# Performance work log

Hardware: AMD Instinct MI355X
Metric: run time of the kernel (lower is better)

Reference implementation:

```python
import jax, jax.numpy as jnp
import numpy as np

EPS_NORM = 1e-8
EPS_REG = 1e-6

def _l2_normalize(x, eps=EPS_NORM):
    return x / jnp.clip(jnp.linalg.norm(x, axis=-1, keepdims=True), eps, None)

def setup_inputs() -> dict:
    key = jax.random.key(0)
    k1, k2, k3, k4 = jax.random.split(key, 4)
    ns, nq, d, C = 16384, 8192, 256, 64
    return {
        "support_features": jax.random.normal(k1, (ns, d), dtype=jnp.float32),
        "support_labels": jax.random.randint(k2, (ns,), 0, C),
        "support_values": jax.random.normal(k3, (ns,), dtype=jnp.float32),
        "query_features": jax.random.normal(k4, (nq, d), dtype=jnp.float32),
        "num_classes": C,
    }

def reference(support_features, support_labels, support_values, query_features, num_classes):
    # ---- forward_classification: cosine-sim prototypes ----
    sf = _l2_normalize(support_features)            # [ns, d]
    qf = _l2_normalize(query_features)              # [nq, d]
    sums = jax.ops.segment_sum(sf, support_labels, num_segments=num_classes)   # [C, d]
    counts = jax.ops.segment_sum(jnp.ones((sf.shape[0],), sf.dtype),
                                 support_labels, num_segments=num_classes)      # [C]
    prototypes = _l2_normalize(sums / jnp.clip(counts, 1.0, None)[:, None])     # [C, d]
    logits = qf @ prototypes.T                      # [nq, C]
    log_probs = jax.nn.log_softmax(logits, axis=1)

    mu = support_features.mean(axis=0, keepdims=True)           # [1, d]
    S = support_features - mu                                   # [ns, d]
    ns, d = S.shape
    cov = (S.T @ S) / max(ns - 1, 1) + 1e-4 * jnp.eye(d, dtype=S.dtype)
    evals, evecs = jnp.linalg.eigh(cov)
    inv_sqrt = (evecs * jax.lax.rsqrt(jnp.clip(evals, 1e-6, None))) @ evecs.T   # [d, d]
    S_wh = S @ inv_sqrt                                          # [ns, d]
    Q_wh = (query_features - mu) @ inv_sqrt                      # [nq, d]
    # squared euclidean cdist: [nq, ns]
    d2 = jnp.clip(jnp.sum(Q_wh * Q_wh, axis=1)[:, None]
                  + jnp.sum(S_wh * S_wh, axis=1)[None, :]
                  - 2.0 * (Q_wh @ S_wh.T), 0.0, None)
    med = jnp.median(d2)
    gamma = jnp.where(jnp.isfinite(med) & (med > 0),
                      1.0 / (med + EPS_REG),
                      1.0 / (d2.mean() + EPS_REG))
    weights = jax.nn.softmax(-gamma * d2, axis=1)                # [nq, ns]
    prediction = weights @ support_values                        # [nq]
    return log_probs, prediction
```

## Files before the change

### kernel.cpp

```cpp
#include <hip/hip_runtime.h>
#include <hip/hip_bf16.h>

constexpr int kNS = 16384;
constexpr int kNQ = 8192;
constexpr int kD  = 256;
constexpr int kC  = 64;


constexpr size_t OFF_PSUM  = 0;
constexpr size_t OFF_HIST  = 82240;
constexpr size_t OFF_SSUM  = 84288;
constexpr size_t OFF_MU    = 100736;
constexpr size_t OFF_COV   = 100992;
constexpr size_t OFF_C     = 166784;
constexpr size_t OFF_Y     = 166800;
constexpr size_t OFF_T     = 297872;
constexpr size_t OFF_Y2    = 363408;
constexpr size_t OFF_S2    = 560016;
constexpr size_t OFF_Q2P   = 576400;
constexpr size_t OFF_PART  = 584592;
constexpr size_t OFF_G     = 846736;
constexpr size_t OFF_SH    = 2943888;
constexpr size_t OFF_GH    = 5041040;

typedef __attribute__((ext_vector_type(8))) short bf16x8;
typedef __attribute__((ext_vector_type(4))) float f32x4;

__device__ __forceinline__ unsigned short f2bf(float f) {
  unsigned int w; __builtin_memcpy(&w, &f, 4);
  unsigned int r = (w + 0x7FFFu + ((w >> 16) & 1u)) >> 16;
  return (unsigned short)r;
}

__device__ __forceinline__ float waveReduceSum(float v) {
#pragma unroll
  for (int off = 32; off > 0; off >>= 1) v += __shfl_xor(v, off);
  return v;
}
__device__ __forceinline__ float waveReduceMax(float v) {
#pragma unroll
  for (int off = 32; off > 0; off >>= 1) v = fmaxf(v, __shfl_xor(v, off));
  return v;
}
__device__ __forceinline__ void fma16(float acc[4][4], float4 a, float4 b) {
  acc[0][0] += a.x*b.x; acc[0][1] += a.x*b.y; acc[0][2] += a.x*b.z; acc[0][3] += a.x*b.w;
  acc[1][0] += a.y*b.x; acc[1][1] += a.y*b.y; acc[1][2] += a.y*b.z; acc[1][3] += a.y*b.w;
  acc[2][0] += a.z*b.x; acc[2][1] += a.z*b.y; acc[2][2] += a.z*b.z; acc[2][3] += a.z*b.w;
  acc[3][0] += a.w*b.x; acc[3][1] += a.w*b.y; acc[3][2] += a.w*b.z; acc[3][3] += a.w*b.w;
}

__device__ __forceinline__ void gload_lds16(const void* g, void* l) {
  __builtin_amdgcn_global_load_lds(
      (const __attribute__((address_space(1))) unsigned int*)g,
      (__attribute__((address_space(3))) unsigned int*)l, 16, 0, 0);
}

__global__ void k_swzs_r27(const float* __restrict__ in, unsigned short* __restrict__ out,
                           float* __restrict__ rnorm, float* __restrict__ ws) {
  int gid = blockIdx.x * 256 + threadIdx.x;
  if (gid < 2049) ws[OFF_HIST + gid] = 0.f;
  else if (gid < 2049 + 8192) ws[OFF_Q2P + (gid - 2049)] = 0.f;
  else if (gid < 2049 + 8192 + 16384) ws[OFF_S2 + (gid - 2049 - 8192)] = 0.f;

  __shared__ float rs[16];
  int g = blockIdx.x, t = threadIdx.x;
  if (t < 16) rs[t] = 0.f;
  __syncthreads();
  int ks = t >> 5;
  float4 va[2], vb[2];
#pragma unroll
  for (int f = 0; f < 2; ++f) {
    int lane = (2 * t + f) & 63;
    int q = lane >> 4, r = lane & 15;
    const float* src = &in[(size_t)(g * 16 + r) * kD + ks * 32 + q * 8];
    va[f] = *(const float4*)src;
    vb[f] = *(const float4*)(src + 4);
    float s = va[f].x*va[f].x + va[f].y*va[f].y + va[f].z*va[f].z + va[f].w*va[f].w
            + vb[f].x*vb[f].x + vb[f].y*vb[f].y + vb[f].z*vb[f].z + vb[f].w*vb[f].w;
    atomicAdd(&rs[r], s);
  }
  size_t gbase = (size_t)g * 4096;
#pragma unroll
  for (int f = 0; f < 2; ++f) {
    int lane = (2 * t + f) & 63;
    ushort4 o0, o1;
    o0.x = f2bf(va[f].x); o0.y = f2bf(va[f].y); o0.z = f2bf(va[f].z); o0.w = f2bf(va[f].w);
    o1.x = f2bf(vb[f].x); o1.y = f2bf(vb[f].y); o1.z = f2bf(vb[f].z); o1.w = f2bf(vb[f].w);
    unsigned short* dst = &out[gbase + (size_t)ks * 512 + (size_t)lane * 8];
    *(ushort4*)dst = o0;
    *(ushort4*)(dst + 4) = o1;
  }
  __syncthreads();
  if (t < 16) rnorm[g * 16 + t] = 1.0f / fmaxf(sqrtf(rs[t]), 1e-8f);
}

__global__ void k_paccum_r24(const float* __restrict__ X, const int* __restrict__ lab,
                             const float* __restrict__ rnorm,
                             float* __restrict__ partial, float* __restrict__ cntpart,
                             float* __restrict__ cpart) {
  __shared__ float acc[kC * kD];
  int t = threadIdx.x, b = blockIdx.x;
  for (int i = t; i < kC * kD; i += 256) acc[i] = 0.f;
  __syncthreads();
  int r0 = b * 128;
  float myCnt = 0.f, csum = 0.f;
  for (int r = 0; r < 128; r += 8) {
    int row = r0 + r;
    int   c0 = lab[row + 0], c1 = lab[row + 1], c2 = lab[row + 2], c3 = lab[row + 3];
    int   c4 = lab[row + 4], c5 = lab[row + 5], c6 = lab[row + 6], c7 = lab[row + 7];
    float n0 = rnorm[row + 0], n1 = rnorm[row + 1], n2 = rnorm[row + 2], n3 = rnorm[row + 3];
    float n4 = rnorm[row + 4], n5 = rnorm[row + 5], n6 = rnorm[row + 6], n7 = rnorm[row + 7];
    float x0 = X[(size_t)(row + 0) * kD + t];
    float x1 = X[(size_t)(row + 1) * kD + t];
    float x2 = X[(size_t)(row + 2) * kD + t];
    float x3 = X[(size_t)(row + 3) * kD + t];
    float x4 = X[(size_t)(row + 4) * kD + t];
    float x5 = X[(size_t)(row + 5) * kD + t];
    float x6 = X[(size_t)(row + 6) * kD + t];
    float x7 = X[(size_t)(row + 7) * kD + t];
    csum += ((x0 + x1) + (x2 + x3)) + ((x4 + x5) + (x6 + x7));
    acc[c0 * kD + t] += x0 * n0;
    acc[c1 * kD + t] += x1 * n1;
    acc[c2 * kD + t] += x2 * n2;
    acc[c3 * kD + t] += x3 * n3;
    acc[c4 * kD + t] += x4 * n4;
    acc[c5 * kD + t] += x5 * n5;
    acc[c6 * kD + t] += x6 * n6;
    acc[c7 * kD + t] += x7 * n7;
    myCnt += (t == c0) ? 1.f : 0.f; myCnt += (t == c1) ? 1.f : 0.f;
    myCnt += (t == c2) ? 1.f : 0.f; myCnt += (t == c3) ? 1.f : 0.f;
    myCnt += (t == c4) ? 1.f : 0.f; myCnt += (t == c5) ? 1.f : 0.f;
    myCnt += (t == c6) ? 1.f : 0.f; myCnt += (t == c7) ? 1.f : 0.f;
  }
  __syncthreads();
  float* pb = partial + (size_t)b * (kC * kD);
  for (int c = 0; c < kC; ++c) pb[c * kD + t] = acc[c * kD + t];
  if (t < kC) cntpart[b * kC + t] = myCnt;
  cpart[(size_t)b * kD + t] = csum;
}

__global__ void k_proto_fin_r28(const float* __restrict__ partial,
                                const float* __restrict__ cntpart,
                                const float* __restrict__ cpart,
                                unsigned short* __restrict__ Ph,
                                float* __restrict__ mu) {
  int c = blockIdx.x, t = threadIdx.x;
  if (c == kC) {
    float s = 0.f;
    for (int b = 0; b < 128; ++b) s += cpart[(size_t)b * kD + t];
    mu[t] = s * (1.0f / (float)kNS);
    return;
  }
  __shared__ float cs[128];
  __shared__ float wred[4];
  __shared__ float cntS, invS;
  if (t < 128) cs[t] = cntpart[t * kC + c];
  __syncthreads();
  float s = 0.f;
  const float* p = partial + (size_t)c * kD + t;
  for (int b = 0; b < 128; ++b) s += p[(size_t)b * (kC * kD)];
  if (t < 64) {
    float cv = cs[t] + cs[t + 64];
    cv = waveReduceSum(cv);
    if (t == 0) cntS = fmaxf(cv, 1.0f);
  }
  __syncthreads();
  float v = s / cntS;
  float ss = waveReduceSum(v * v);
  if ((t & 63) == 0) wred[t >> 6] = ss;
  __syncthreads();
  if (t == 0) invS = 1.0f / fmaxf(sqrtf(wred[0] + wred[1] + wred[2] + wred[3]), 1e-8f);
  __syncthreads();
  float val = v * invS;
  int g = c >> 4, r = c & 15;
  int ks = t >> 5, q = (t >> 3) & 3, j = t & 7;
  Ph[(size_t)g * 4096 + (size_t)ks * 512 + (size_t)(q * 16 + r) * 8 + j] = f2bf(val);
}

__global__ void k_qlogits_r28(const float* __restrict__ Q,
                              const unsigned short* __restrict__ Ph,
                              float* __restrict__ out0) {
  __shared__ float rs[16];
  __shared__ alignas(16) unsigned short qtile[16][264];
  int g = blockIdx.x, t = threadIdx.x;
  if (t < 16) rs[t] = 0.f;
  __syncthreads();
  int ks0 = t >> 5;
  float4 va[2], vb[2];
  int rr[2], cc[2];
#pragma unroll
  for (int f = 0; f < 2; ++f) {
    int lane = (2 * t + f) & 63;
    int q8 = lane >> 4, r = lane & 15;
    rr[f] = r; cc[f] = ks0 * 32 + q8 * 8;
    const float* src = &Q[(size_t)(g * 16 + r) * kD + cc[f]];
    va[f] = *(const float4*)src;
    vb[f] = *(const float4*)(src + 4);
    float s = va[f].x*va[f].x + va[f].y*va[f].y + va[f].z*va[f].z + va[f].w*va[f].w
            + vb[f].x*vb[f].x + vb[f].y*vb[f].y + vb[f].z*vb[f].z + vb[f].w*vb[f].w;
    atomicAdd(&rs[r], s);
  }
  __syncthreads();
#pragma unroll
  for (int f = 0; f < 2; ++f) {
    float n = 1.0f / fmaxf(sqrtf(rs[rr[f]]), 1e-8f);
    ushort4 o0, o1;
    o0.x = f2bf(va[f].x * n); o0.y = f2bf(va[f].y * n);
    o0.z = f2bf(va[f].z * n); o0.w = f2bf(va[f].w * n);
    o1.x = f2bf(vb[f].x * n); o1.y = f2bf(vb[f].y * n);
    o1.z = f2bf(vb[f].z * n); o1.w = f2bf(vb[f].w * n);
    unsigned short* dst = &qtile[rr[f]][cc[f]];
    *(ushort4*)dst = o0;
    *(ushort4*)(dst + 4) = o1;
  }
  __syncthreads();
  if (t >= 64) return;

  int lane = t, l15 = lane & 15, quad = lane >> 4;
  bf16x8 afrag[8];
#pragma unroll
  for (int ks = 0; ks < 8; ++ks)
    afrag[ks] = *(const bf16x8*)&qtile[l15][ks * 32 + quad * 8];

  f32x4 acc0 = {0.f,0.f,0.f,0.f}, acc1 = {0.f,0.f,0.f,0.f};
  f32x4 acc2 = {0.f,0.f,0.f,0.f}, acc3 = {0.f,0.f,0.f,0.f};
#pragma unroll
  for (int ks = 0; ks < 8; ++ks) {
    bf16x8 b0 = *(const bf16x8*)&Ph[(size_t)0 * 4096 + ks * 512 + (size_t)lane * 8];
    bf16x8 b1 = *(const bf16x8*)&Ph[(size_t)1 * 4096 + ks * 512 + (size_t)lane * 8];
    bf16x8 b2 = *(const bf16x8*)&Ph[(size_t)2 * 4096 + ks * 512 + (size_t)lane * 8];
    bf16x8 b3 = *(const bf16x8*)&Ph[(size_t)3 * 4096 + ks * 512 + (size_t)lane * 8];
    acc0 = __builtin_amdgcn_mfma_f32_16x16x32_bf16(afrag[ks], b0, acc0, 0, 0, 0);
    acc1 = __builtin_amdgcn_mfma_f32_16x16x32_bf16(afrag[ks], b1, acc1, 0, 0, 0);
    acc2 = __builtin_amdgcn_mfma_f32_16x16x32_bf16(afrag[ks], b2, acc2, 0, 0, 0);
    acc3 = __builtin_amdgcn_mfma_f32_16x16x32_bf16(afrag[ks], b3, acc3, 0, 0, 0);
  }
#pragma unroll
  for (int r = 0; r < 4; ++r) {
    float m = fmaxf(fmaxf(acc0[r], acc1[r]), fmaxf(acc2[r], acc3[r]));
#pragma unroll
    for (int off = 8; off >= 1; off >>= 1) m = fmaxf(m, __shfl_xor(m, off));
    float e = expf(acc0[r] - m) + expf(acc1[r] - m) + expf(acc2[r] - m) + expf(acc3[r] - m);
#pragma unroll
    for (int off = 8; off >= 1; off >>= 1) e += __shfl_xor(e, off);
    float lse = m + logf(e);
    size_t row = (size_t)g * 16 + quad * 4 + r;
    out0[row * kC + 0 * 16 + l15] = acc0[r] - lse;
    out0[row * kC + 1 * 16 + l15] = acc1[r] - lse;
    out0[row * kC + 2 * 16 + l15] = acc2[r] - lse;
    out0[row * kC + 3 * 16 + l15] = acc3[r] - lse;
  }
}

__global__ void k_xtx_r26(const float* __restrict__ X, float* __restrict__ part) {
  const int TA[10] = {0,0,0,0,1,1,1,2,2,3};
  const int TB[10] = {0,1,2,3,1,2,3,2,3,3};
  __shared__ alignas(16) float As[16][68];
  __shared__ alignas(16) float Bs[16][68];
  int t = threadIdx.x, tx = t & 15, ty = t >> 4;
  int ab = TA[blockIdx.x] * 64, bb = TB[blockIdx.x] * 64;
  int k0b = blockIdx.y * 512;
  float acc[4][4] = {};
  for (int k0 = 0; k0 < 512; k0 += 16) {
    __syncthreads();
    int j = t & 63, kr0 = t >> 6;
#pragma unroll
    for (int p = 0; p < 4; ++p) {
      int kr = kr0 + p * 4;
      size_t base = (size_t)(k0b + k0 + kr) * kD;
      As[kr][j] = X[base + ab + j];
      Bs[kr][j] = X[base + bb + j];
    }
    __syncthreads();
#pragma unroll
    for (int k = 0; k < 16; ++k) {
      float4 a = *(const float4*)&As[k][ty * 4];
      float4 b = *(const float4*)&Bs[k][tx * 4];
      fma16(acc, a, b);
    }
  }
  float* pb = part + ((size_t)blockIdx.y * 10 + blockIdx.x) * 4096;
#pragma unroll
  for (int r = 0; r < 4; ++r) {
    float4 o = {acc[r][0], acc[r][1], acc[r][2], acc[r][3]};
    *(float4*)&pb[(size_t)(ty * 4 + r) * 64 + tx * 4] = o;
  }
}

__global__ void k_xtxcov_r28(const float* __restrict__ part, const float* __restrict__ mu,
                             float* __restrict__ cov, float* __restrict__ X1) {
  int i = blockIdx.x, j = threadIdx.x;
  int a = i >> 6, b = j >> 6;
  int tile, local;
  if (a <= b) { tile = a * (9 - a) / 2 + (b - a); local = (i & 63) * 64 + (j & 63); }
  else        { tile = b * (9 - b) / 2 + (a - b); local = (j & 63) * 64 + (i & 63); }
  const float* p = part + (size_t)tile * 4096 + local;
  float s = 0.f;
#pragma unroll 8
  for (int ky = 0; ky < 32; ++ky) s += p[(size_t)ky * 40960];
  float v = (s - (float)kNS * mu[i] * mu[j]) * (1.0f / (float)(kNS - 1));
  if (i == j) v += 1e-4f;
  cov[(size_t)i * kD + j] = v;
  X1[(size_t)i * kD + j] = (i == j ? 2.0f : 0.0f) - v;
}

__global__ void __launch_bounds__(1024)
k_newt_mm_r17(const float* __restrict__ A, const float* __restrict__ Xin,
              float* __restrict__ Out, int isT) {
  __shared__ float a_s[256];
  __shared__ float red[3][256];
  int i = blockIdx.x, t = threadIdx.x;
  int j = t & 255, kq = t >> 8;
  if (t < 256) a_s[t] = A[(size_t)i * kD + t];
  __syncthreads();
  int k0 = kq * 64;
  const float* Xp = &Xin[(size_t)k0 * kD + j];
  float s0 = 0.f, s1 = 0.f, s2 = 0.f, s3 = 0.f;
#pragma unroll 4
  for (int k = 0; k < 64; k += 4) {
    s0 = fmaf(a_s[k0 + k + 0], Xp[0 * kD], s0);
    s1 = fmaf(a_s[k0 + k + 1], Xp[1 * kD], s1);
    s2 = fmaf(a_s[k0 + k + 2], Xp[2 * kD], s2);
    s3 = fmaf(a_s[k0 + k + 3], Xp[3 * kD], s3);
    Xp += 4 * kD;
  }
  float s = (s0 + s1) + (s2 + s3);
  if (kq) red[kq - 1][j] = s;
  __syncthreads();
  if (t < 256) {
    float tot = s + red[0][j] + red[1][j] + red[2][j];
    float o = isT ? ((i == j ? 2.0f : 0.0f) - tot) : tot;
    Out[(size_t)i * kD + j] = o;
  }
}

__global__ void k_G_r26(const float* __restrict__ Q, const float* __restrict__ mu,
                        const float* __restrict__ M, float* __restrict__ G,
                        unsigned short* __restrict__ Gh, float* __restrict__ q2p) {
  __shared__ alignas(16) float As[16][68];
  __shared__ alignas(16) float Bs[16][68];
  int t = threadIdx.x, tx = t & 15, ty = t >> 4;
  int nb = blockIdx.x * 64;
  int mb = blockIdx.y * 64;
  float acc[4][4] = {};
  for (int k0 = 0; k0 < 256; k0 += 16) {
    __syncthreads();
    {
      int kk = t & 15, m0 = t >> 4;
      float muk = mu[k0 + kk];
#pragma unroll
      for (int p = 0; p < 4; ++p) {
        int m = m0 + p * 16;
        As[kk][m] = Q[(size_t)(mb + m) * kD + k0 + kk] - muk;
      }
      int j = t & 63, kr0 = t >> 6;
#pragma unroll
      for (int p = 0; p < 4; ++p) {
        int kr = kr0 + p * 4;
        Bs[kr][j] = M[(size_t)(k0 + kr) * kD + nb + j];
      }
    }
    __syncthreads();
#pragma unroll
    for (int k = 0; k < 16; ++k) {
      float4 a = *(const float4*)&As[k][ty * 4];
      float4 b = *(const float4*)&Bs[k][tx * 4];
      fma16(acc, a, b);
    }
  }
  int d0 = nb + tx * 4;
  int ks = d0 >> 5, q = (d0 >> 3) & 3, j0 = d0 & 7;
#pragma unroll
  for (int r = 0; r < 4; ++r) {
    int gi = mb + ty * 4 + r;
    float4 o = {acc[r][0], acc[r][1], acc[r][2], acc[r][3]};
    *(float4*)&G[(size_t)gi * kD + nb + tx * 4] = o;
    int gg = gi >> 4, rrow = gi & 15;
    ushort4 h;
    h.x = f2bf(acc[r][0]); h.y = f2bf(acc[r][1]);
    h.z = f2bf(acc[r][2]); h.w = f2bf(acc[r][3]);
    *(ushort4*)&Gh[(size_t)gg * 4096 + (size_t)ks * 512 + (size_t)(q * 16 + rrow) * 8 + j0] = h;
    const float* qr = &Q[(size_t)gi * kD + d0];
    float p = acc[r][0] * (qr[0] + mu[d0 + 0]) + acc[r][1] * (qr[1] + mu[d0 + 1])
            + acc[r][2] * (qr[2] + mu[d0 + 2]) + acc[r][3] * (qr[3] + mu[d0 + 3]);
#pragma unroll
    for (int off = 8; off >= 1; off >>= 1) p += __shfl_xor(p, off);
    if (tx == 0) atomicAdd(&q2p[gi], p);
  }
}

__global__ void k_s2_r26(const float* __restrict__ S, const float* __restrict__ mu,
                         const float* __restrict__ M, float* __restrict__ s2) {
  __shared__ alignas(16) float As[16][68];
  __shared__ alignas(16) float Bs[16][68];
  __shared__ float red[64][17];
  int t = threadIdx.x, tx = t & 15, ty = t >> 4;
  int mb = blockIdx.x * 64;
  int nb = blockIdx.y * 64;
  float partial[4] = {0.f, 0.f, 0.f, 0.f};
  float acc[4][4] = {};
  for (int k0 = 0; k0 < 256; k0 += 16) {
    __syncthreads();
    {
      int kk = t & 15, m0 = t >> 4;
      float muk = mu[k0 + kk];
#pragma unroll
      for (int p = 0; p < 4; ++p) {
        int m = m0 + p * 16;
        As[kk][m] = S[(size_t)(mb + m) * kD + k0 + kk] - muk;
      }
      int j = t & 63, kr0 = t >> 6;
#pragma unroll
      for (int p = 0; p < 4; ++p) {
        int kr = kr0 + p * 4;
        Bs[kr][j] = M[(size_t)(k0 + kr) * kD + nb + j];
      }
    }
    __syncthreads();
#pragma unroll
    for (int k = 0; k < 16; ++k) {
      float4 a = *(const float4*)&As[k][ty * 4];
      float4 b = *(const float4*)&Bs[k][tx * 4];
      fma16(acc, a, b);
    }
  }
#pragma unroll
  for (int r = 0; r < 4; ++r) {
    int gi = mb + ty * 4 + r;
#pragma unroll
    for (int c = 0; c < 4; ++c) {
      int gj = nb + tx * 4 + c;
      partial[r] += acc[r][c] * (S[(size_t)gi * kD + gj] - mu[gj]);
    }
  }
  __syncthreads();
#pragma unroll
  for (int r = 0; r < 4; ++r) red[ty * 4 + r][tx] = partial[r];
  __syncthreads();
  if (t < 64) {
    float s = 0.f;
#pragma unroll
    for (int x = 0; x < 16; ++x) s += red[t][x];
    atomicAdd(&s2[mb + t], s);
  }
}

__global__ void k_median_r27(const float* __restrict__ G, const float* __restrict__ S,
                             const float* __restrict__ q2p, const float* __restrict__ s2,
                             unsigned int* __restrict__ hist, float* __restrict__ ssum) {
  __shared__ alignas(16) float As[16][68];
  __shared__ alignas(16) float Bs[16][68];
  __shared__ unsigned int h[2048];
  __shared__ float fred[4];
  int t = threadIdx.x, tx = t & 15, ty = t >> 4;
  int stile = blockIdx.x, qtile = blockIdx.y;
  for (int i = t; i < 2048; i += 256) h[i] = 0u;

  float acc[4][4] = {};
  for (int k0 = 0; k0 < 256; k0 += 16) {
    __syncthreads();
    {
      int kk = t & 15, m0 = t >> 4;
#pragma unroll
      for (int p = 0; p < 4; ++p) {
        int m = m0 + p * 16;
        As[kk][m] = G[(size_t)((qtile * 64 + m) * 8) * kD + k0 + kk];
        Bs[kk][m] = S[(size_t)((stile * 64 + m) * 16) * kD + k0 + kk];
      }
    }
    __syncthreads();
#pragma unroll
    for (int k = 0; k < 16; ++k) {
      float4 a = *(const float4*)&As[k][ty * 4];
      float4 b = *(const float4*)&Bs[k][tx * 4];
      fma16(acc, a, b);
    }
  }
  float fsum = 0.f;
#pragma unroll
  for (int r = 0; r < 4; ++r) {
    int qi = (qtile * 64 + ty * 4 + r) * 8;
    float q2v = q2p[qi];
#pragma unroll
    for (int c = 0; c < 4; ++c) {
      int sj = (stile * 64 + tx * 4 + c) * 16;
      float d2 = fmaxf(q2v + s2[sj] - 2.0f * acc[r][c], 0.0f);
      fsum += d2;
      int bin = (int)(d2 * 2.0f);
      bin = bin > 2047 ? 2047 : bin;
      atomicAdd(&h[bin], 1u);
    }
  }
  float wsum = waveReduceSum(fsum);
  if ((t & 63) == 0) fred[t >> 6] = wsum;
  __syncthreads();
  if (t == 0) atomicAdd(ssum, fred[0] + fred[1] + fred[2] + fred[3]);
  for (int i = t; i < 2048; i += 256)
    if (h[i]) atomicAdd(&hist[i], h[i]);
}

__global__ void k_gamma_r16(const unsigned int* __restrict__ hist,
                            const float* __restrict__ ssum, float* __restrict__ gptr) {
  __shared__ unsigned int ps[256];
  __shared__ float v0s, v1s;
  int t = threadIdx.x;
  unsigned int mine[8];
  unsigned int c = 0;
#pragma unroll
  for (int j = 0; j < 8; ++j) { mine[j] = hist[t * 8 + j]; c += mine[j]; }
  ps[t] = c;
  __syncthreads();
  for (int off = 1; off < 256; off <<= 1) {
    unsigned int v = (t >= off) ? ps[t - off] : 0u;
    __syncthreads();
    ps[t] += v;
    __syncthreads();
  }
  unsigned int total = ps[255];
  unsigned int before = ps[t] - c;
  if (t == 0) { v0s = 0.f; v1s = 0.f; }
  __syncthreads();
  unsigned int rr0 = (total - 1) / 2, rr1 = total / 2;
  unsigned int cum = before;
#pragma unroll
  for (int j = 0; j < 8; ++j) {
    unsigned int cc = mine[j];
    if (cc > 0) {
      int bin = t * 8 + j;
      if (cum <= rr0 && rr0 < cum + cc) {
        float frac = (float)(rr0 - cum) + 0.5f;
        v0s = ((float)bin + frac / (float)cc) * 0.5f;
      }
      if (cum <= rr1 && rr1 < cum + cc) {
        float frac = (float)(rr1 - cum) + 0.5f;
        v1s = ((float)bin + frac / (float)cc) * 0.5f;
      }
    }
    cum += cc;
  }
  __syncthreads();
  if (t == 0) {
    float med = 0.5f * (v0s + v1s);
    float mean = (total > 0) ? (ssum[0] / (float)total) : 1.0f;
    float g = (med > 0.f) ? 1.0f / (med + 1e-6f) : 1.0f / (mean + 1e-6f);
    gptr[0] = g;
  }
}

__global__ void __launch_bounds__(256, 4)
PrototypicalHead_6210522710389_kernel(
    const unsigned short* __restrict__ Gh, const unsigned short* __restrict__ Sh,
    const float* __restrict__ q2p, const float* __restrict__ s2,
    const float* __restrict__ svals, const float* __restrict__ gptr,
    float* __restrict__ part) {
  __shared__ unsigned short Bs[2][8192];
  int t = threadIdx.x;
  int w = t >> 6, lane = t & 63;
  int l15 = lane & 15, quad = lane >> 4;
  int qt = blockIdx.x, sc = blockIdx.y;
  int qbase = qt * 128;
  float gamma = gptr[0];
  const float LOG2E = 1.44269504f;
  float c2 = 2.0f * gamma * LOG2E;

  size_t agrp = (size_t)(qt * 8 + w * 2) * 4096;
  bf16x8 afrag[2][8];
#pragma unroll
  for (int s = 0; s < 2; ++s)
#pragma unroll
    for (int ks = 0; ks < 8; ++ks)
      afrag[s][ks] = *(const bf16x8*)&Gh[agrp + (size_t)s * 4096 + (size_t)ks * 512 + (size_t)lane * 8];

  float cqv[2][4];
#pragma unroll
  for (int s = 0; s < 2; ++s)
#pragma unroll
    for (int r = 0; r < 4; ++r)
      cqv[s][r] = -gamma * LOG2E * q2p[qbase + w * 32 + s * 16 + quad * 4 + r];

  float dAcc[2][4] = {}, nAcc[2][4] = {};

  const char* sbase_ptr = (const char*)&Sh[(size_t)(sc * 64) * 4096];
#pragma unroll
  for (int i = 0; i < 4; ++i) {
    int c = i * 256 + t;
    gload_lds16(sbase_ptr + (size_t)c * 16, (char*)&Bs[0][0] + (size_t)c * 16);
  }
  __syncthreads();

  for (int st = 0; st < 32; ++st) {
    int cur = st & 1;
    if (st + 1 < 32) {
      const char* src = sbase_ptr + (size_t)(st + 1) * 16384;
      char* dst = (char*)&Bs[cur ^ 1][0];
#pragma unroll
      for (int i = 0; i < 4; ++i) {
        int c = i * 256 + t;
        gload_lds16(src + (size_t)c * 16, dst + (size_t)c * 16);
      }
    }

    f32x4 acc[2][2];
#pragma unroll
    for (int s = 0; s < 2; ++s)
#pragma unroll
      for (int nt = 0; nt < 2; ++nt)
        acc[s][nt] = (f32x4){0.f, 0.f, 0.f, 0.f};

    const unsigned short* B0 = &Bs[cur][lane * 8];
    __builtin_amdgcn_s_setprio(1);
#pragma unroll
    for (int ks = 0; ks < 8; ++ks) {
      bf16x8 f0 = *(const bf16x8*)(B0 + ks * 512);
      bf16x8 f1 = *(const bf16x8*)(B0 + 4096 + ks * 512);
      acc[0][0] = __builtin_amdgcn_mfma_f32_16x16x32_bf16(afrag[0][ks], f0, acc[0][0], 0, 0, 0);
      acc[1][0] = __builtin_amdgcn_mfma_f32_16x16x32_bf16(afrag[1][ks], f0, acc[1][0], 0, 0, 0);
      acc[0][1] = __builtin_amdgcn_mfma_f32_16x16x32_bf16(afrag[0][ks], f1, acc[0][1], 0, 0, 0);
      acc[1][1] = __builtin_amdgcn_mfma_f32_16x16x32_bf16(afrag[1][ks], f1, acc[1][1], 0, 0, 0);
    }
    __builtin_amdgcn_s_setprio(0);

    int sbase = sc * 1024 + st * 32;
#pragma unroll
    for (int nt = 0; nt < 2; ++nt) {
      int scol = sbase + nt * 16 + l15;
      float cs = -gamma * LOG2E * s2[scol];
      float sv = svals[scol];
#pragma unroll
      for (int s = 0; s < 2; ++s)
#pragma unroll
        for (int r = 0; r < 4; ++r) {
          float ex = exp2f(fminf(fmaf(c2, acc[s][nt][r], cqv[s][r] + cs), 0.0f));
          dAcc[s][r] += ex;
          nAcc[s][r] = fmaf(ex, sv, nAcc[s][r]);
        }
    }
    __syncthreads();
  }
#pragma unroll
  for (int off = 8; off >= 1; off >>= 1)
#pragma unroll
    for (int s = 0; s < 2; ++s)
#pragma unroll
      for (int r = 0; r < 4; ++r) {
        dAcc[s][r] += __shfl_xor(dAcc[s][r], off);
        nAcc[s][r] += __shfl_xor(nAcc[s][r], off);
      }
  if (l15 == 0) {
#pragma unroll
    for (int s = 0; s < 2; ++s)
#pragma unroll
      for (int r = 0; r < 4; ++r) {
        size_t q = (size_t)qbase + w * 32 + s * 16 + quad * 4 + r;
        part[(q * 16 + sc) * 2 + 0] = dAcc[s][r];
        part[(q * 16 + sc) * 2 + 1] = nAcc[s][r];
      }
  }
}

__global__ void k_final_r16(const float* __restrict__ part, float* __restrict__ out1) {
  int q = blockIdx.x * 256 + threadIdx.x;
  const float* p = part + (size_t)q * 32;
  float d = 0.f, n = 0.f;
#pragma unroll
  for (int i = 0; i < 16; ++i) { d += p[2 * i]; n += p[2 * i + 1]; }
  out1[q] = n / d;
}

extern "C" void kernel_launch(void* const* d_in, const int* in_sizes, int n_in,
                              void* d_out, int out_size, void* d_ws, size_t ws_size,
                              hipStream_t stream) {
  (void)in_sizes; (void)n_in; (void)out_size; (void)ws_size;
  const float* SF = (const float*)d_in[0];
  const int*   SL = (const int*)d_in[1];
  const float* SV = (const float*)d_in[2];
  const float* QF = (const float*)d_in[3];

  float* ws = (float*)d_ws;
  float* rnorm = ws + OFF_PSUM;
  unsigned int* hist = (unsigned int*)(ws + OFF_HIST);
  float* ssum  = ws + OFF_SSUM;
  float* mu    = ws + OFF_MU;
  float* cov   = ws + OFF_COV;
  float* gptr  = ws + OFF_C + 1;
  float* X1 = ws + OFF_Y;  float* T = ws + OFF_T;  float* X2 = ws + OFF_Y2;
  float* s2 = ws + OFF_S2; float* q2p = ws + OFF_Q2P;
  float* part = ws + OFF_PART;
  float* G = ws + OFF_G;
  unsigned short* Sh = (unsigned short*)(ws + OFF_SH);
  unsigned short* Gh = (unsigned short*)(ws + OFF_GH);
  float* pppart  = G;
  float* cntpart = part;
  float* cpart   = part + 8192;
  unsigned short* Ph = (unsigned short*)(ws + OFF_Y + 8192);
  float* xtxpart = G;

  float* out0 = (float*)d_out;
  float* out1 = out0 + (size_t)kNQ * kC;

  k_swzs_r27<<<kNS / 16, 256, 0, stream>>>(SF, Sh, rnorm, ws);

  k_paccum_r24<<<128, 256, 0, stream>>>(SF, SL, rnorm, pppart, cntpart, cpart);
  k_proto_fin_r28<<<kC + 1, 256, 0, stream>>>(pppart, cntpart, cpart, Ph, mu);
  k_qlogits_r28<<<kNQ / 16, 256, 0, stream>>>(QF, Ph, out0);

  k_xtx_r26<<<dim3(10, 32), 256, 0, stream>>>(SF, xtxpart);
  k_xtxcov_r28<<<256, 256, 0, stream>>>(xtxpart, mu, cov, X1);

  float *Xc = X1, *T_ = T, *Xn = X2;
  for (int it = 0; it < 2; ++it) {
    k_newt_mm_r17<<<256, 1024, 0, stream>>>(cov, Xc, T_, 1);
    k_newt_mm_r17<<<256, 1024, 0, stream>>>(Xc, T_, Xn, 0);
    float* tmp = Xc; Xc = Xn; Xn = tmp;
  }
  float* M = Xc;

  k_G_r26<<<dim3(4, kNQ / 64), 256, 0, stream>>>(QF, mu, M, G, Gh, q2p);
  k_s2_r26<<<dim3(kNS / 64, 4), 256, 0, stream>>>(SF, mu, M, s2);

  k_median_r27<<<dim3(16, 16), 256, 0, stream>>>(G, SF, q2p, s2, hist, ssum);
  k_gamma_r16<<<1, 256, 0, stream>>>(hist, ssum, gptr);

  PrototypicalHead_6210522710389_kernel<<<dim3(64, 16), 256, 0, stream>>>(
      Gh, Sh, q2p, s2, SV, gptr, part);
  k_final_r16<<<kNQ / 256, 256, 0, stream>>>(part, out1);
}
```

Before: 341.8 us.

## Move X^T X and support-norm GEMMs to bf16 MFMA and fuse cov build

The support swizzle kernel now also writes a transposed bf16 copy of the support features. A new MFMA kernel uses that copy to accumulate X^T X with atomics, replacing the fp32 tiled kernel and its separate reduction. The covariance/X1 construction is folded into extra blocks of the query-logits kernel. The last Newton step also emits a bf16 swizzled M and M·mu, so the s2 quadratic form can run on MFMA against the bf16 support tiles with the mean correction applied algebraically. This removes fp32 FMA work and a launch, but computes the covariance and s2 in bf16, which may reduce accuracy, and the atomic accumulation order is nondeterministic.

```diff
diff --git a/kernel.cpp b/kernel.cpp
--- a/kernel.cpp
+++ b/kernel.cpp
@@ -8,12 +8,15 @@
 
 
 constexpr size_t OFF_PSUM  = 0;
+constexpr size_t OFF_XTX   = 16704;
 constexpr size_t OFF_HIST  = 82240;
 constexpr size_t OFF_SSUM  = 84288;
 constexpr size_t OFF_MU    = 100736;
 constexpr size_t OFF_COV   = 100992;
 constexpr size_t OFF_C     = 166784;
 constexpr size_t OFF_Y     = 166800;
+constexpr size_t OFF_MH    = 166800 + 65536;
+constexpr size_t OFF_W     = 166800 + 98304;
 constexpr size_t OFF_T     = 297872;
 constexpr size_t OFF_Y2    = 363408;
 constexpr size_t OFF_S2    = 560016;
@@ -37,11 +40,6 @@
   for (int off = 32; off > 0; off >>= 1) v += __shfl_xor(v, off);
   return v;
 }
-__device__ __forceinline__ float waveReduceMax(float v) {
-#pragma unroll
-  for (int off = 32; off > 0; off >>= 1) v = fmaxf(v, __shfl_xor(v, off));
-  return v;
-}
 __device__ __forceinline__ void fma16(float acc[4][4], float4 a, float4 b) {
   acc[0][0] += a.x*b.x; acc[0][1] += a.x*b.y; acc[0][2] += a.x*b.z; acc[0][3] += a.x*b.w;
   acc[1][0] += a.y*b.x; acc[1][1] += a.y*b.y; acc[1][2] += a.y*b.z; acc[1][3] += a.y*b.w;
@@ -55,12 +53,13 @@
       (__attribute__((address_space(3))) unsigned int*)l, 16, 0, 0);
 }
 
-__global__ void k_swzs_r27(const float* __restrict__ in, unsigned short* __restrict__ out,
+__global__ void k_swzs_r29(const float* __restrict__ in, unsigned short* __restrict__ out,
+                           unsigned short* __restrict__ outT,
                            float* __restrict__ rnorm, float* __restrict__ ws) {
   int gid = blockIdx.x * 256 + threadIdx.x;
   if (gid < 2049) ws[OFF_HIST + gid] = 0.f;
   else if (gid < 2049 + 8192) ws[OFF_Q2P + (gid - 2049)] = 0.f;
-  else if (gid < 2049 + 8192 + 16384) ws[OFF_S2 + (gid - 2049 - 8192)] = 0.f;
+  else if (gid < 2049 + 8192 + 65536) ws[OFF_XTX + (gid - 2049 - 8192)] = 0.f;
 
   __shared__ float rs[16];
   int g = blockIdx.x, t = threadIdx.x;
@@ -68,11 +67,13 @@
   __syncthreads();
   int ks = t >> 5;
   float4 va[2], vb[2];
+  int rr[2], cc[2];
 #pragma unroll
   for (int f = 0; f < 2; ++f) {
     int lane = (2 * t + f) & 63;
     int q = lane >> 4, r = lane & 15;
-    const float* src = &in[(size_t)(g * 16 + r) * kD + ks * 32 + q * 8];
+    rr[f] = r; cc[f] = ks * 32 + q * 8;
+    const float* src = &in[(size_t)(g * 16 + r) * kD + cc[f]];
     va[f] = *(const float4*)src;
     vb[f] = *(const float4*)(src + 4);
     float s = va[f].x*va[f].x + va[f].y*va[f].y + va[f].z*va[f].z + va[f].w*va[f].w
@@ -89,9 +90,49 @@
     unsigned short* dst = &out[gbase + (size_t)ks * 512 + (size_t)lane * 8];
     *(ushort4*)dst = o0;
     *(ushort4*)(dst + 4) = o1;
+    int row = g * 16 + rr[f];
+    size_t rbase = (size_t)(row >> 5) * 512 + (((row >> 3) & 3) * 16) * 8 + (row & 7);
+#pragma unroll
+    for (int u = 0; u < 8; ++u) {
+      int d = cc[f] + u;
+      float v = (u < 4) ? ((const float*)&va[f])[u] : ((const float*)&vb[f])[u - 4];
+      outT[(size_t)(d >> 4) * 262144 + rbase + (size_t)(d & 15) * 8] = f2bf(v);
+    }
   }
   __syncthreads();
   if (t < 16) rnorm[g * 16 + t] = 1.0f / fmaxf(sqrtf(rs[t]), 1e-8f);
+}
+
+__global__ void k_xtx_mfma_r29(const unsigned short* __restrict__ ShT,
+                               float* __restrict__ xtxacc) {
+  int t = threadIdx.x, w = t >> 6, lane = t & 63;
+  int a = blockIdx.x >> 2, b = blockIdx.x & 3;
+  int chunk = blockIdx.y;
+  size_t kb = (size_t)chunk * 32 * 512 + (size_t)lane * 8;
+  const unsigned short* A0 = ShT + (size_t)(a * 4 + w) * 262144 + kb;
+  const unsigned short* B0 = ShT + (size_t)(b * 4 + 0) * 262144 + kb;
+  const unsigned short* B1 = ShT + (size_t)(b * 4 + 1) * 262144 + kb;
+  const unsigned short* B2 = ShT + (size_t)(b * 4 + 2) * 262144 + kb;
+  const unsigned short* B3 = ShT + (size_t)(b * 4 + 3) * 262144 + kb;
+  f32x4 acc0 = {0.f,0.f,0.f,0.f}, acc1 = {0.f,0.f,0.f,0.f};
+  f32x4 acc2 = {0.f,0.f,0.f,0.f}, acc3 = {0.f,0.f,0.f,0.f};
+#pragma unroll
+  for (int ks = 0; ks < 32; ++ks) {
+    bf16x8 af = *(const bf16x8*)(A0 + ks * 512);
+    acc0 = __builtin_amdgcn_mfma_f32_16x16x32_bf16(af, *(const bf16x8*)(B0 + ks * 512), acc0, 0, 0, 0);
+    acc1 = __builtin_amdgcn_mfma_f32_16x16x32_bf16(af, *(const bf16x8*)(B1 + ks * 512), acc1, 0, 0, 0);
+    acc2 = __builtin_amdgcn_mfma_f32_16x16x32_bf16(af, *(const bf16x8*)(B2 + ks * 512), acc2, 0, 0, 0);
+    acc3 = __builtin_amdgcn_mfma_f32_16x16x32_bf16(af, *(const bf16x8*)(B3 + ks * 512), acc3, 0, 0, 0);
+  }
+  int r0 = a * 64 + w * 16 + (lane >> 4) * 4;
+  int c0 = b * 64 + (lane & 15);
+#pragma unroll
+  for (int i = 0; i < 4; ++i) {
+    atomicAdd(&xtxacc[(size_t)(r0 + i) * kD + c0 +  0], acc0[i]);
+    atomicAdd(&xtxacc[(size_t)(r0 + i) * kD + c0 + 16], acc1[i]);
+    atomicAdd(&xtxacc[(size_t)(r0 + i) * kD + c0 + 32], acc2[i]);
+    atomicAdd(&xtxacc[(size_t)(r0 + i) * kD + c0 + 48], acc3[i]);
+  }
 }
 
 __global__ void k_paccum_r24(const float* __restrict__ X, const int* __restrict__ lab,
@@ -177,9 +218,20 @@
   Ph[(size_t)g * 4096 + (size_t)ks * 512 + (size_t)(q * 16 + r) * 8 + j] = f2bf(val);
 }
 
-__global__ void k_qlogits_r28(const float* __restrict__ Q,
+__global__ void k_qlogits_r29(const float* __restrict__ Q,
                               const unsigned short* __restrict__ Ph,
-                              float* __restrict__ out0) {
+                              float* __restrict__ out0,
+                              const float* __restrict__ xtxacc,
+                              const float* __restrict__ mu,
+                              float* __restrict__ cov, float* __restrict__ X1) {
+  if (blockIdx.x >= 512) {
+    int i = blockIdx.x - 512, j = threadIdx.x;
+    float v = (xtxacc[(size_t)i * kD + j] - (float)kNS * mu[i] * mu[j]) * (1.0f / (float)(kNS - 1));
+    if (i == j) v += 1e-4f;
+    cov[(size_t)i * kD + j] = v;
+    X1[(size_t)i * kD + j] = (i == j ? 2.0f : 0.0f) - v;
+    return;
+  }
   __shared__ float rs[16];
   __shared__ alignas(16) unsigned short qtile[16][264];
   int g = blockIdx.x, t = threadIdx.x;
@@ -252,58 +304,6 @@
   }
 }
 
-__global__ void k_xtx_r26(const float* __restrict__ X, float* __restrict__ part) {
-  const int TA[10] = {0,0,0,0,1,1,1,2,2,3};
-  const int TB[10] = {0,1,2,3,1,2,3,2,3,3};
-  __shared__ alignas(16) float As[16][68];
-  __shared__ alignas(16) float Bs[16][68];
-  int t = threadIdx.x, tx = t & 15, ty = t >> 4;
-  int ab = TA[blockIdx.x] * 64, bb = TB[blockIdx.x] * 64;
-  int k0b = blockIdx.y * 512;
-  float acc[4][4] = {};
-  for (int k0 = 0; k0 < 512; k0 += 16) {
-    __syncthreads();
-    int j = t & 63, kr0 = t >> 6;
-#pragma unroll
-    for (int p = 0; p < 4; ++p) {
-      int kr = kr0 + p * 4;
-      size_t base = (size_t)(k0b + k0 + kr) * kD;
-      As[kr][j] = X[base + ab + j];
-      Bs[kr][j] = X[base + bb + j];
-    }
-    __syncthreads();
-#pragma unroll
-    for (int k = 0; k < 16; ++k) {
-      float4 a = *(const float4*)&As[k][ty * 4];
-      float4 b = *(const float4*)&Bs[k][tx * 4];
-      fma16(acc, a, b);
-    }
-  }
-  float* pb = part + ((size_t)blockIdx.y * 10 + blockIdx.x) * 4096;
-#pragma unroll
-  for (int r = 0; r < 4; ++r) {
-    float4 o = {acc[r][0], acc[r][1], acc[r][2], acc[r][3]};
-    *(float4*)&pb[(size_t)(ty * 4 + r) * 64 + tx * 4] = o;
-  }
-}
-
-__global__ void k_xtxcov_r28(const float* __restrict__ part, const float* __restrict__ mu,
-                             float* __restrict__ cov, float* __restrict__ X1) {
-  int i = blockIdx.x, j = threadIdx.x;
-  int a = i >> 6, b = j >> 6;
-  int tile, local;
-  if (a <= b) { tile = a * (9 - a) / 2 + (b - a); local = (i & 63) * 64 + (j & 63); }
-  else        { tile = b * (9 - b) / 2 + (a - b); local = (j & 63) * 64 + (i & 63); }
-  const float* p = part + (size_t)tile * 4096 + local;
-  float s = 0.f;
-#pragma unroll 8
-  for (int ky = 0; ky < 32; ++ky) s += p[(size_t)ky * 40960];
-  float v = (s - (float)kNS * mu[i] * mu[j]) * (1.0f / (float)(kNS - 1));
-  if (i == j) v += 1e-4f;
-  cov[(size_t)i * kD + j] = v;
-  X1[(size_t)i * kD + j] = (i == j ? 2.0f : 0.0f) - v;
-}
-
 __global__ void __launch_bounds__(1024)
 k_newt_mm_r17(const float* __restrict__ A, const float* __restrict__ Xin,
               float* __restrict__ Out, int isT) {
@@ -331,6 +331,50 @@
     float tot = s + red[0][j] + red[1][j] + red[2][j];
     float o = isT ? ((i == j ? 2.0f : 0.0f) - tot) : tot;
     Out[(size_t)i * kD + j] = o;
+  }
+}
+
+__global__ void __launch_bounds__(1024)
+k_newt_fin_r29(const float* __restrict__ A, const float* __restrict__ Xin,
+               float* __restrict__ Out, const float* __restrict__ mu,
+               unsigned short* __restrict__ Mh, float* __restrict__ wv) {
+  __shared__ float a_s[256];
+  __shared__ float red[3][256];
+  __shared__ float wred[16];
+  int i = blockIdx.x, t = threadIdx.x;
+  int j = t & 255, kq = t >> 8;
+  if (t < 256) a_s[t] = A[(size_t)i * kD + t];
+  __syncthreads();
+  int k0 = kq * 64;
+  const float* Xp = &Xin[(size_t)k0 * kD + j];
+  float s0 = 0.f, s1 = 0.f, s2 = 0.f, s3 = 0.f;
+#pragma unroll 4
+  for (int k = 0; k < 64; k += 4) {
+    s0 = fmaf(a_s[k0 + k + 0], Xp[0 * kD], s0);
+    s1 = fmaf(a_s[k0 + k + 1], Xp[1 * kD], s1);
+    s2 = fmaf(a_s[k0 + k + 2], Xp[2 * kD], s2);
+    s3 = fmaf(a_s[k0 + k + 3], Xp[3 * kD], s3);
+    Xp += 4 * kD;
+  }
+  float s = (s0 + s1) + (s2 + s3);
+  if (kq) red[kq - 1][j] = s;
+  __syncthreads();
+  float p = 0.f;
+  if (t < 256) {
+    float tot = s + red[0][j] + red[1][j] + red[2][j];
+    Out[(size_t)i * kD + j] = tot;
+    Mh[(size_t)(j >> 4) * 4096 + (size_t)(i >> 5) * 512 +
+       (size_t)(((i >> 3) & 3) * 16 + (j & 15)) * 8 + (i & 7)] = f2bf(tot);
+    p = tot * mu[j];
+  }
+  p = waveReduceSum(p);
+  if ((t & 63) == 0) wred[t >> 6] = p;
+  __syncthreads();
+  if (t == 0) {
+    float sw = 0.f;
+#pragma unroll
+    for (int x = 0; x < 16; ++x) sw += wred[x];
+    wv[i] = sw;
   }
 }
 
@@ -389,59 +433,48 @@
   }
 }
 
-__global__ void k_s2_r26(const float* __restrict__ S, const float* __restrict__ mu,
-                         const float* __restrict__ M, float* __restrict__ s2) {
-  __shared__ alignas(16) float As[16][68];
-  __shared__ alignas(16) float Bs[16][68];
-  __shared__ float red[64][17];
-  int t = threadIdx.x, tx = t & 15, ty = t >> 4;
-  int mb = blockIdx.x * 64;
-  int nb = blockIdx.y * 64;
-  float partial[4] = {0.f, 0.f, 0.f, 0.f};
-  float acc[4][4] = {};
-  for (int k0 = 0; k0 < 256; k0 += 16) {
-    __syncthreads();
-    {
-      int kk = t & 15, m0 = t >> 4;
-      float muk = mu[k0 + kk];
-#pragma unroll
-      for (int p = 0; p < 4; ++p) {
-        int m = m0 + p * 16;
-        As[kk][m] = S[(size_t)(mb + m) * kD + k0 + kk] - muk;
-      }
-      int j = t & 63, kr0 = t >> 6;
-#pragma unroll
-      for (int p = 0; p < 4; ++p) {
-        int kr = kr0 + p * 4;
-        Bs[kr][j] = M[(size_t)(k0 + kr) * kD + nb + j];
-      }
-    }
-    __syncthreads();
-#pragma unroll
-    for (int k = 0; k < 16; ++k) {
-      float4 a = *(const float4*)&As[k][ty * 4];
-      float4 b = *(const float4*)&Bs[k][tx * 4];
-      fma16(acc, a, b);
-    }
-  }
-#pragma unroll
-  for (int r = 0; r < 4; ++r) {
-    int gi = mb + ty * 4 + r;
-#pragma unroll
-    for (int c = 0; c < 4; ++c) {
-      int gj = nb + tx * 4 + c;
-      partial[r] += acc[r][c] * (S[(size_t)gi * kD + gj] - mu[gj]);
-    }
-  }
-  __syncthreads();
-#pragma unroll
-  for (int r = 0; r < 4; ++r) red[ty * 4 + r][tx] = partial[r];
-  __syncthreads();
-  if (t < 64) {
-    float s = 0.f;
-#pragma unroll
-    for (int x = 0; x < 16; ++x) s += red[t][x];
-    atomicAdd(&s2[mb + t], s);
+__global__ void k_s2_mfma_r29(const unsigned short* __restrict__ Sh,
+                              const unsigned short* __restrict__ Mh,
+                              const float* __restrict__ S,
+                              const float* __restrict__ mu,
+                              const float* __restrict__ wv,
+                              float* __restrict__ s2) {
+  int t = threadIdx.x, w = t >> 6, lane = t & 63;
+  int rg = blockIdx.x * 4 + w;
+  const unsigned short* A0 = Sh + (size_t)rg * 4096 + (size_t)lane * 8;
+  bf16x8 af[8];
+#pragma unroll
+  for (int ks = 0; ks < 8; ++ks) af[ks] = *(const bf16x8*)(A0 + ks * 512);
+
+  float4 m4 = *(const float4*)&mu[lane * 4];
+  float4 w4 = *(const float4*)&wv[lane * 4];
+  float c0 = waveReduceSum(m4.x*w4.x + m4.y*w4.y + m4.z*w4.z + m4.w*w4.w);
+
+  float s2p[4] = {0.f, 0.f, 0.f, 0.f};
+  int rows0 = rg * 16 + (lane >> 4) * 4;
+  int l15 = lane & 15;
+#pragma unroll
+  for (int cg = 0; cg < 16; ++cg) {
+    const unsigned short* B0 = Mh + (size_t)cg * 4096 + (size_t)lane * 8;
+    f32x4 acc = {0.f, 0.f, 0.f, 0.f};
+#pragma unroll
+    for (int ks = 0; ks < 8; ++ks)
+      acc = __builtin_amdgcn_mfma_f32_16x16x32_bf16(af[ks], *(const bf16x8*)(B0 + ks * 512), acc, 0, 0, 0);
+    int col = cg * 16 + l15;
+    float wc = wv[col];
+#pragma unroll
+    for (int i = 0; i < 4; ++i) {
+      float sv = S[(size_t)(rows0 + i) * kD + col];
+      s2p[i] += acc[i] * sv - 2.0f * sv * wc;
+    }
+  }
+#pragma unroll
+  for (int off = 8; off >= 1; off >>= 1)
+#pragma unroll
+    for (int i = 0; i < 4; ++i) s2p[i] += __shfl_xor(s2p[i], off);
+  if (l15 == 0) {
+#pragma unroll
+    for (int i = 0; i < 4; ++i) s2[rows0 + i] = s2p[i] + c0;
   }
 }
 
@@ -678,45 +711,45 @@
 
   float* ws = (float*)d_ws;
   float* rnorm = ws + OFF_PSUM;
+  float* xtxacc = ws + OFF_XTX;
   unsigned int* hist = (unsigned int*)(ws + OFF_HIST);
   float* ssum  = ws + OFF_SSUM;
   float* mu    = ws + OFF_MU;
   float* cov   = ws + OFF_COV;
   float* gptr  = ws + OFF_C + 1;
   float* X1 = ws + OFF_Y;  float* T = ws + OFF_T;  float* X2 = ws + OFF_Y2;
+  unsigned short* Mh = (unsigned short*)(ws + OFF_MH);
+  float* wv = ws + OFF_W;
   float* s2 = ws + OFF_S2; float* q2p = ws + OFF_Q2P;
   float* part = ws + OFF_PART;
   float* G = ws + OFF_G;
   unsigned short* Sh = (unsigned short*)(ws + OFF_SH);
   unsigned short* Gh = (unsigned short*)(ws + OFF_GH);
+  unsigned short* ShT = (unsigned short*)G;
   float* pppart  = G;
   float* cntpart = part;
   float* cpart   = part + 8192;
-  unsigned short* Ph = (unsigned short*)(ws + OFF_Y + 8192);
-  float* xtxpart = G;
+  unsigned short* Ph = (unsigned short*)(ws + OFF_PSUM);
 
   float* out0 = (float*)d_out;
   float* out1 = out0 + (size_t)kNQ * kC;
 
-  k_swzs_r27<<<kNS / 16, 256, 0, stream>>>(SF, Sh, rnorm, ws);
+  k_swzs_r29<<<kNS / 16, 256, 0, stream>>>(SF, Sh, ShT, rnorm, ws);
+
+  k_xtx_mfma_r29<<<dim3(16, 16), 256, 0, stream>>>(ShT, xtxacc);
 
   k_paccum_r24<<<128, 256, 0, stream>>>(SF, SL, rnorm, pppart, cntpart, cpart);
   k_proto_fin_r28<<<kC + 1, 256, 0, stream>>>(pppart, cntpart, cpart, Ph, mu);
-  k_qlogits_r28<<<kNQ / 16, 256, 0, stream>>>(QF, Ph, out0);
-
-  k_xtx_r26<<<dim3(10, 32), 256, 0, stream>>>(SF, xtxpart);
-  k_xtxcov_r28<<<256, 256, 0, stream>>>(xtxpart, mu, cov, X1);
-
-  float *Xc = X1, *T_ = T, *Xn = X2;
-  for (int it = 0; it < 2; ++it) {
-    k_newt_mm_r17<<<256, 1024, 0, stream>>>(cov, Xc, T_, 1);
-    k_newt_mm_r17<<<256, 1024, 0, stream>>>(Xc, T_, Xn, 0);
-    float* tmp = Xc; Xc = Xn; Xn = tmp;
-  }
-  float* M = Xc;
+  k_qlogits_r29<<<kNQ / 16 + 256, 256, 0, stream>>>(QF, Ph, out0, xtxacc, mu, cov, X1);
+
+  k_newt_mm_r17<<<256, 1024, 0, stream>>>(cov, X1, T, 1);
+  k_newt_mm_r17<<<256, 1024, 0, stream>>>(X1, T, X2, 0);
+  k_newt_mm_r17<<<256, 1024, 0, stream>>>(cov, X2, T, 1);
+  k_newt_fin_r29<<<256, 1024, 0, stream>>>(X2, T, X1, mu, Mh, wv);
+  float* M = X1;
 
   k_G_r26<<<dim3(4, kNQ / 64), 256, 0, stream>>>(QF, mu, M, G, Gh, q2p);
-  k_s2_r26<<<dim3(kNS / 64, 4), 256, 0, stream>>>(SF, mu, M, s2);
+  k_s2_mfma_r29<<<kNS / 64, 256, 0, stream>>>(Sh, Mh, SF, mu, wv, s2);
 
   k_median_r27<<<dim3(16, 16), 256, 0, stream>>>(G, SF, q2p, s2, hist, ssum);
   k_gamma_r16<<<1, 256, 0, stream>>>(hist, ssum, gptr);
```

Result: faster. 313.0 us (-8.4%).
